# Kernel optimization log

Hardware: AMD Instinct MI355X
Metric: run time of the kernel (lower is better)

Reference implementation:

```python
import jax, jax.numpy as jnp
import numpy as np

N_NODES = 500_000
N_EDGES = 16_000_000
N_LAYERS = 49
ALPHA = 0.3  # GCN2Conv alpha; beta = 1.0 (no theta/layer given)

# per-layer activation applied AFTER the conv (layer index 0-based)
_LEAKY = {1, 11, 21, 31, 41}
_SIG = {4, 14, 24, 34, 44}


def setup_inputs() -> dict:
    key = jax.random.key(0)
    k1, k2, k3 = jax.random.split(key, 3)
    x = jax.random.normal(k1, (N_NODES, 1), dtype=jnp.float32)
    adj = jax.random.randint(k2, (2, N_EDGES), 0, N_NODES, dtype=jnp.int64)
    # 49 scalar (1x1) layer weights
    w = jax.random.normal(k3, (N_LAYERS,), dtype=jnp.float32) * 0.1
    return {"input": x, "w": w, "adj": adj}


def _gcn_norm(adj, n):
    # add self-loops, symmetric normalization D^-1/2 (A+I) D^-1/2
    loops = jnp.arange(n, dtype=adj.dtype)
    src = jnp.concatenate([adj[0], loops])
    dst = jnp.concatenate([adj[1], loops])
    deg = jax.ops.segment_sum(jnp.ones(src.shape[0], jnp.float32), dst, num_segments=n)
    dis = 1.0 / jnp.sqrt(deg)  # deg >= 1 due to self-loops
    ew = dis[src] * dis[dst]
    return src, dst, ew


def reference(input, w, adj):
    n = input.shape[0]
    x0 = input.astype(jnp.float32)
    src, dst, ew = _gcn_norm(adj, n)
    ewc = ew[:, None]  # [E+N, 1]

    def gcn2(x, wl):
        h = jax.ops.segment_sum(ewc * x[src], dst, num_segments=n)  # A_hat @ x
        comb = (1.0 - ALPHA) * h + ALPHA * x0                       # residual mix
        return comb * wl                                            # 1x1 weight, beta=1

    x = x0
    for i in range(N_LAYERS):
        y = gcn2(x, w[i])
        if i == 0:
            x = y  # no activation after gcn1
        elif i == N_LAYERS - 1:
            x = n * jax.nn.sigmoid(y)  # CustomSigmoid: len(x) * sigmoid(x)
        elif i in _LEAKY:
            x = jax.nn.leaky_relu(y, 0.01)
        elif i in _SIG:
            x = jax.nn.sigmoid(y)
        else:
            x = jax.nn.relu(y)
        # dropout(p=0.0) is identity
    return jnp.squeeze(x, 1).astype(jnp.int64)
```

## Files before the change

kernel.cpp:

```cpp
#include <hip/hip_runtime.h>
#include <math.h>

#define NN 500000
#define NE 16000000
#define NBKT 1954
#define PB 16384
#define NPB_BLOCKS ((NE + PB - 1) / PB)
#define BKT_CAP 9216

__global__ __launch_bounds__(256) void hist_kernel(const int4* __restrict__ dst4,
                                                   int* __restrict__ bcnt) {
    __shared__ int lh[NBKT];
    for (int i = threadIdx.x; i < NBKT; i += 256) lh[i] = 0;
    __syncthreads();
    long base4 = (long)blockIdx.x * (PB / 4);
    for (int k = 0; k < PB / 4; k += 256) {
        long i4 = base4 + k + threadIdx.x;
        if (i4 < NE / 4) {
            int4 d = dst4[i4];
            atomicAdd(&lh[d.x >> 8], 1);
            atomicAdd(&lh[d.y >> 8], 1);
            atomicAdd(&lh[d.z >> 8], 1);
            atomicAdd(&lh[d.w >> 8], 1);
        }
    }
    __syncthreads();
    for (int i = threadIdx.x; i < NBKT; i += 256) {
        int c = lh[i];
        if (c) atomicAdd(&bcnt[i], c);
    }
}

__global__ __launch_bounds__(256) void scan_buckets(int* __restrict__ bcnt,
                                                    int* __restrict__ bbase) {
    __shared__ int sh[256];
    __shared__ int carry_sh;
    if (threadIdx.x == 0) carry_sh = 0;
    __syncthreads();
    for (int base = 0; base < NBKT; base += 256) {
        int i = base + threadIdx.x;
        int v = (i < NBKT) ? bcnt[i] : 0;
        sh[threadIdx.x] = v;
        __syncthreads();
        for (int off = 1; off < 256; off <<= 1) {
            int t = (threadIdx.x >= off) ? sh[threadIdx.x - off] : 0;
            __syncthreads();
            sh[threadIdx.x] += t;
            __syncthreads();
        }
        int incl = sh[threadIdx.x];
        int c = carry_sh;
        __syncthreads();
        if (i < NBKT) {
            int ex = c + incl - v;
            bbase[i] = ex;
            bcnt[i] = ex;
        }
        if (threadIdx.x == 255) carry_sh = c + incl;
        __syncthreads();
    }
    if (threadIdx.x == 0) bbase[NBKT] = NE;
}

__global__ __launch_bounds__(256) void partition_kernel(const int* __restrict__ src,
                                                        const int* __restrict__ dst,
                                                        int* __restrict__ bcur,
                                                        int* __restrict__ ebuf) {
    __shared__ int lh[NBKT];
    for (int i = threadIdx.x; i < NBKT; i += 256) lh[i] = 0;
    __syncthreads();
    long base = (long)blockIdx.x * PB;
    for (int k = 0; k < PB; k += 256) {
        long e = base + k + threadIdx.x;
        if (e < NE) atomicAdd(&lh[dst[e] >> 8], 1);
    }
    __syncthreads();
    for (int i = threadIdx.x; i < NBKT; i += 256) {
        int c = lh[i];
        if (c) lh[i] = atomicAdd(&bcur[i], c);
    }
    __syncthreads();
    for (int k = 0; k < PB; k += 256) {
        long e = base + k + threadIdx.x;
        if (e < NE) {
            int d = dst[e];
            int pos = atomicAdd(&lh[d >> 8], 1);
            ebuf[pos] = ((d & 255) << 19) | src[e];
        }
    }
}

__global__ __launch_bounds__(256) void bucket_csr(const int* __restrict__ bbase,
                                                  int* __restrict__ ebuf,
                                                  int* __restrict__ rp,
                                                  float* __restrict__ dis) {
    __shared__ int eds[BKT_CAP];
    __shared__ int cnt[256];
    __shared__ int scn[256];
    int b = blockIdx.x;
    int ebase = bbase[b];
    int nb = bbase[b + 1] - ebase;
    if (nb > BKT_CAP) nb = BKT_CAP;
    for (int i = threadIdx.x; i < nb; i += 256) eds[i] = ebuf[ebase + i];
    cnt[threadIdx.x] = 0;
    __syncthreads();
    for (int i = threadIdx.x; i < nb; i += 256) atomicAdd(&cnt[eds[i] >> 19], 1);
    __syncthreads();
    int my = cnt[threadIdx.x];
    scn[threadIdx.x] = my;
    __syncthreads();
    for (int off = 1; off < 256; off <<= 1) {
        int t = (threadIdx.x >= off) ? scn[threadIdx.x - off] : 0;
        __syncthreads();
        scn[threadIdx.x] += t;
        __syncthreads();
    }
    int excl = scn[threadIdx.x] - my;
    int v = b * 256 + threadIdx.x;
    if (v < NN) {
        rp[v] = ebase + excl;
        dis[v] = rsqrtf((float)(my + 1));
    }
    __syncthreads();
    cnt[threadIdx.x] = excl;
    __syncthreads();
    for (int i = threadIdx.x; i < nb; i += 256) {
        int p = eds[i];
        int pos = atomicAdd(&cnt[p >> 19], 1);
        ebuf[ebase + pos] = p & 0x7FFFF;
    }
    if (b == 0 && threadIdx.x == 0) rp[NN] = NE;
}

__global__ void init_z(const float* __restrict__ x0, const float* __restrict__ dis,
                       float* __restrict__ z) {
    int i = blockIdx.x * 256 + threadIdx.x;
    if (i < NN) z[i] = x0[i] * dis[i];
}

__global__ __launch_bounds__(256) void layer_kernel(
        const int* __restrict__ rp, const int* __restrict__ csr,
        const float* __restrict__ zin, const float* __restrict__ dis,
        const float* __restrict__ x0, const float* __restrict__ w,
        int li, int act, float* __restrict__ zout, int* __restrict__ out) {
    int tid = blockIdx.x * 256 + threadIdx.x;
    int v = tid >> 3;
    int lane = threadIdx.x & 7;
    int beg = rp[v];
    int end = rp[v + 1];
    float s = 0.f;
    for (int j = beg + lane; j < end; j += 8) s += zin[csr[j]];
    s += __shfl_xor(s, 1);
    s += __shfl_xor(s, 2);
    s += __shfl_xor(s, 4);
    if (lane != 0) return;
    s += zin[v];
    float h = dis[v] * s;
    float comb = 0.7f * h + 0.3f * x0[v];
    float y = comb * w[li];
    if (act == 4) {
        float sg = 1.f / (1.f + expf(-y));
        out[v] = (int)(500000.f * sg);
        return;
    }
    float r;
    if (act == 0)      r = y;
    else if (act == 1) r = fmaxf(y, 0.f);
    else if (act == 2) r = (y > 0.f) ? y : 0.01f * y;
    else               r = 1.f / (1.f + expf(-y));
    zout[v] = dis[v] * r;
}

extern "C" void kernel_launch(void* const* d_in, const int* in_sizes, int n_in,
                              void* d_out, int out_size, void* d_ws, size_t ws_size,
                              hipStream_t stream) {
    const float* x0  = (const float*)d_in[0];
    const float* w   = (const float*)d_in[1];
    const int*   adj = (const int*)d_in[2];
    const int*   src = adj;
    const int*   dst = adj + NE;
    int* out = (int*)d_out;

    uintptr_t p = (uintptr_t)d_ws;
    auto alloc = [&](size_t bytes) -> void* {
        p = (p + 255) & ~(uintptr_t)255;
        void* r = (void*)p;
        p += bytes;
        return r;
    };
    float* dis   = (float*)alloc((size_t)NN * 4);
    int*   rp    = (int*)alloc((size_t)(NN + 1) * 4);
    float* z0    = (float*)alloc((size_t)NN * 4);
    float* z1    = (float*)alloc((size_t)NN * 4);
    int*   bcnt  = (int*)alloc((size_t)NBKT * 4);
    int*   bbase = (int*)alloc((size_t)(NBKT + 1) * 4);
    int*   csr   = (int*)alloc((size_t)NE * 4);
    (void)ws_size;

    hipMemsetAsync(bcnt, 0, (size_t)NBKT * 4, stream);

    hist_kernel<<<NPB_BLOCKS, 256, 0, stream>>>((const int4*)dst, bcnt);
    scan_buckets<<<1, 256, 0, stream>>>(bcnt, bbase);
    partition_kernel<<<NPB_BLOCKS, 256, 0, stream>>>(src, dst, bcnt, csr);
    bucket_csr<<<NBKT, 256, 0, stream>>>(bbase, csr, rp, dis);
    init_z<<<(NN + 255) / 256, 256, 0, stream>>>(x0, dis, z0);

    float* zbuf[2] = {z0, z1};
    const int LB = (NN * 8) / 256;
    for (int i = 0; i < 49; i++) {
        int act;
        if (i == 0)            act = 0;
        else if (i == 48)      act = 4;
        else if (i % 10 == 1)  act = 2;
        else if (i % 10 == 4)  act = 3;
        else                   act = 1;
        layer_kernel<<<LB, 256, 0, stream>>>(rp, csr, zbuf[i & 1], dis, x0, w,
                                             i, act, zbuf[(i + 1) & 1], out);
    }
}
```

Measured before the change: 4.477 ms.

## Enlarge partition blocks, vectorize edge loads, stage CSR writes, unroll gathers

```diff
diff --git a/kernel.cpp b/kernel.cpp
--- a/kernel.cpp
+++ b/kernel.cpp
@@ -4,17 +4,17 @@
 #define NN 500000
 #define NE 16000000
 #define NBKT 1954
-#define PB 16384
-#define NPB_BLOCKS ((NE + PB - 1) / PB)
+#define PB2 65536
+#define NPB2 ((NE + PB2 - 1) / PB2)
 #define BKT_CAP 9216
 
-__global__ __launch_bounds__(256) void hist_kernel(const int4* __restrict__ dst4,
-                                                   int* __restrict__ bcnt) {
+__global__ __launch_bounds__(1024) void hist_kernel(const int4* __restrict__ dst4,
+                                                    int* __restrict__ bcnt) {
     __shared__ int lh[NBKT];
-    for (int i = threadIdx.x; i < NBKT; i += 256) lh[i] = 0;
-    __syncthreads();
-    long base4 = (long)blockIdx.x * (PB / 4);
-    for (int k = 0; k < PB / 4; k += 256) {
+    for (int i = threadIdx.x; i < NBKT; i += 1024) lh[i] = 0;
+    __syncthreads();
+    long base4 = (long)blockIdx.x * (PB2 / 4);
+    for (int k = 0; k < PB2 / 4; k += 1024) {
         long i4 = base4 + k + threadIdx.x;
         if (i4 < NE / 4) {
             int4 d = dst4[i4];
@@ -25,7 +25,7 @@
         }
     }
     __syncthreads();
-    for (int i = threadIdx.x; i < NBKT; i += 256) {
+    for (int i = threadIdx.x; i < NBKT; i += 1024) {
         int c = lh[i];
         if (c) atomicAdd(&bcnt[i], c);
     }
@@ -62,30 +62,40 @@
     if (threadIdx.x == 0) bbase[NBKT] = NE;
 }
 
-__global__ __launch_bounds__(256) void partition_kernel(const int* __restrict__ src,
-                                                        const int* __restrict__ dst,
-                                                        int* __restrict__ bcur,
-                                                        int* __restrict__ ebuf) {
+__global__ __launch_bounds__(1024) void partition_kernel(const int4* __restrict__ src4,
+                                                         const int4* __restrict__ dst4,
+                                                         int* __restrict__ bcur,
+                                                         int* __restrict__ ebuf) {
     __shared__ int lh[NBKT];
-    for (int i = threadIdx.x; i < NBKT; i += 256) lh[i] = 0;
-    __syncthreads();
-    long base = (long)blockIdx.x * PB;
-    for (int k = 0; k < PB; k += 256) {
-        long e = base + k + threadIdx.x;
-        if (e < NE) atomicAdd(&lh[dst[e] >> 8], 1);
-    }
-    __syncthreads();
-    for (int i = threadIdx.x; i < NBKT; i += 256) {
+    for (int i = threadIdx.x; i < NBKT; i += 1024) lh[i] = 0;
+    __syncthreads();
+    long base4 = (long)blockIdx.x * (PB2 / 4);
+    for (int k = 0; k < PB2 / 4; k += 1024) {
+        long i4 = base4 + k + threadIdx.x;
+        if (i4 < NE / 4) {
+            int4 d = dst4[i4];
+            atomicAdd(&lh[d.x >> 8], 1);
+            atomicAdd(&lh[d.y >> 8], 1);
+            atomicAdd(&lh[d.z >> 8], 1);
+            atomicAdd(&lh[d.w >> 8], 1);
+        }
+    }
+    __syncthreads();
+    for (int i = threadIdx.x; i < NBKT; i += 1024) {
         int c = lh[i];
         if (c) lh[i] = atomicAdd(&bcur[i], c);
     }
     __syncthreads();
-    for (int k = 0; k < PB; k += 256) {
-        long e = base + k + threadIdx.x;
-        if (e < NE) {
-            int d = dst[e];
-            int pos = atomicAdd(&lh[d >> 8], 1);
-            ebuf[pos] = ((d & 255) << 19) | src[e];
+    for (int k = 0; k < PB2 / 4; k += 1024) {
+        long i4 = base4 + k + threadIdx.x;
+        if (i4 < NE / 4) {
+            int4 d = dst4[i4];
+            int4 s = src4[i4];
+            int pos;
+            pos = atomicAdd(&lh[d.x >> 8], 1); ebuf[pos] = ((d.x & 255) << 19) | s.x;
+            pos = atomicAdd(&lh[d.y >> 8], 1); ebuf[pos] = ((d.y & 255) << 19) | s.y;
+            pos = atomicAdd(&lh[d.z >> 8], 1); ebuf[pos] = ((d.z & 255) << 19) | s.z;
+            pos = atomicAdd(&lh[d.w >> 8], 1); ebuf[pos] = ((d.w & 255) << 19) | s.w;
         }
     }
 }
@@ -95,6 +105,7 @@
                                                   int* __restrict__ rp,
                                                   float* __restrict__ dis) {
     __shared__ int eds[BKT_CAP];
+    __shared__ int outb[BKT_CAP];
     __shared__ int cnt[256];
     __shared__ int scn[256];
     int b = blockIdx.x;
@@ -127,8 +138,10 @@
     for (int i = threadIdx.x; i < nb; i += 256) {
         int p = eds[i];
         int pos = atomicAdd(&cnt[p >> 19], 1);
-        ebuf[ebase + pos] = p & 0x7FFFF;
-    }
+        outb[pos] = p & 0x7FFFF;
+    }
+    __syncthreads();
+    for (int i = threadIdx.x; i < nb; i += 256) ebuf[ebase + i] = outb[i];
     if (b == 0 && threadIdx.x == 0) rp[NN] = NE;
 }
 
@@ -149,7 +162,19 @@
     int beg = rp[v];
     int end = rp[v + 1];
     float s = 0.f;
-    for (int j = beg + lane; j < end; j += 8) s += zin[csr[j]];
+    int j = beg + lane;
+    for (; j + 24 < end; j += 32) {
+        int c0 = csr[j];
+        int c1 = csr[j + 8];
+        int c2 = csr[j + 16];
+        int c3 = csr[j + 24];
+        float z0 = zin[c0];
+        float z1 = zin[c1];
+        float z2 = zin[c2];
+        float z3 = zin[c3];
+        s += z0; s += z1; s += z2; s += z3;
+    }
+    for (; j < end; j += 8) s += zin[csr[j]];
     s += __shfl_xor(s, 1);
     s += __shfl_xor(s, 2);
     s += __shfl_xor(s, 4);
@@ -199,9 +224,9 @@
 
     hipMemsetAsync(bcnt, 0, (size_t)NBKT * 4, stream);
 
-    hist_kernel<<<NPB_BLOCKS, 256, 0, stream>>>((const int4*)dst, bcnt);
+    hist_kernel<<<NPB2, 1024, 0, stream>>>((const int4*)dst, bcnt);
     scan_buckets<<<1, 256, 0, stream>>>(bcnt, bbase);
-    partition_kernel<<<NPB_BLOCKS, 256, 0, stream>>>(src, dst, bcnt, csr);
+    partition_kernel<<<NPB2, 1024, 0, stream>>>((const int4*)src, (const int4*)dst, bcnt, csr);
     bucket_csr<<<NBKT, 256, 0, stream>>>(bbase, csr, rp, dis);
     init_z<<<(NN + 255) / 256, 256, 0, stream>>>(x0, dis, z0);
 
```

Result: faster. 4.091 ms (-8.6%).
